# Kernel tuning notes

Hardware: AMD Instinct MI355X
Metric: run time of the kernel (lower is better)

The kernel has to match this reference:

```python
import jax, jax.numpy as jnp
import numpy as np

B = 1024      # molecules in batch
M = 128       # atoms per molecule
K = 32        # max_num_neighbors
CUTOFF = 5.0  # radius cutoff


def setup_inputs() -> dict:
    key = jax.random.key(0)
    pos = jax.random.normal(key, (B * M, 3), dtype=jnp.float32) * 3.0
    batch = (jnp.arange(B * M, dtype=jnp.int32) // M).astype(jnp.int32)
    return {"pos": pos, "batch": batch}


def reference(pos, batch):
    # pos: [N,3]; batch is sorted with M atoms per molecule -> reshape [B,M,3]
    p = pos.reshape(B, M, 3)
    sq = jnp.sum(p * p, axis=-1)  # [B,M]
    # per-molecule pairwise squared distances, [B,M,M]
    d2 = sq[:, :, None] + sq[:, None, :] - 2.0 * jnp.einsum('bic,bjc->bij', p, p)
    d2 = jnp.maximum(d2, 0.0)
    valid = d2 < CUTOFF * CUTOFF  # loop=True: self (d2=0) is included
    d2m = jnp.where(valid, d2, jnp.inf)
    neg, idx = jax.lax.top_k(-d2m, K)       # K nearest in-radius, idx: [B,M,K]
    taken = jnp.isfinite(neg)                # which slots are real edges
    local_i = jnp.arange(M, dtype=idx.dtype)
    idx = jnp.where(taken, idx, local_i[None, :, None])  # pad with self index

    # gather neighbor positions: [B,M,K,3]
    p_nb = p[jnp.arange(B)[:, None, None], idx]
    vec = p_nb - p[:, :, None, :]            # pos[edge0] - pos[edge1] (source - target)

    nonself = idx != local_i[None, :, None]
    mask = taken & nonself                   # self-loops & padding get weight 0
    sqv = jnp.sum(vec * vec, axis=-1)
    weight = jnp.where(mask, jnp.sqrt(jnp.where(mask, sqv, 1.0)), 0.0)

    node_base = (jnp.arange(B, dtype=jnp.int32) * M)[:, None, None]
    src = (node_base + idx.astype(jnp.int32)).reshape(-1)                 # edge_index[0] = neighbor j
    dst = jnp.broadcast_to(node_base + local_i.astype(jnp.int32)[None, :, None], (B, M, K)).reshape(-1)
    edge_index = jnp.stack([src, dst], axis=0)          # [2, B*M*K]
    edge_weight = weight.reshape(-1)                    # [B*M*K]
    edge_vec = vec.reshape(-1, 3)                       # [B*M*K, 3]
    return edge_index, edge_weight, edge_vec
```

## Files before the change

### kernel.cpp

```cpp
#include <hip/hip_runtime.h>
#include <stdint.h>

#define BB 1024
#define MM 128
#define KK 32
#define NEDGE (BB * MM * KK)
#define BPB 4
#define ROWS_PER_WAVE (MM / (4 * BPB))

typedef unsigned int uint2v __attribute__((ext_vector_type(2)));

static constexpr unsigned long long p1mask(int size, int stride) {
    unsigned long long m = 0;
    for (int l = 0; l < 64; ++l) {
        int g = l & 31;
        bool up = (((g & size) == 0) != (l >= 32));
        bool keep = (((g & stride) == 0) == up);
        if (keep) m |= 1ull << l;
    }
    return m;
}
static constexpr unsigned long long cleanmask(int stride) {
    unsigned long long m = 0;
    for (int l = 0; l < 64; ++l) {
        int g = l & 31;
        if ((g & stride) == 0) m |= 1ull << l;
    }
    return m;
}

template<int ST, unsigned long long MASK>
static __device__ __forceinline__ unsigned cex(unsigned k) {
    unsigned mn, mx, r;
    if constexpr (ST == 1) {
        asm("s_nop 1\n\t"
            "v_min_u32_dpp %0, %2, %2 quad_perm:[1,0,3,2] row_mask:0xf bank_mask:0xf\n\t"
            "v_max_u32_dpp %1, %2, %2 quad_perm:[1,0,3,2] row_mask:0xf bank_mask:0xf"
            : "=&v"(mn), "=&v"(mx) : "v"(k));
    } else if constexpr (ST == 2) {
        asm("s_nop 1\n\t"
            "v_min_u32_dpp %0, %2, %2 quad_perm:[2,3,0,1] row_mask:0xf bank_mask:0xf\n\t"
            "v_max_u32_dpp %1, %2, %2 quad_perm:[2,3,0,1] row_mask:0xf bank_mask:0xf"
            : "=&v"(mn), "=&v"(mx) : "v"(k));
    } else if constexpr (ST == 8) {
        asm("s_nop 1\n\t"
            "v_min_u32_dpp %0, %2, %2 row_ror:8 row_mask:0xf bank_mask:0xf\n\t"
            "v_max_u32_dpp %1, %2, %2 row_ror:8 row_mask:0xf bank_mask:0xf"
            : "=&v"(mn), "=&v"(mx) : "v"(k));
    } else {
        unsigned p = (unsigned)__builtin_amdgcn_ds_swizzle((int)k, (ST << 10) | 0x1F);
        mn = __builtin_elementwise_min(k, p);
        mx = __builtin_elementwise_max(k, p);
    }
    asm("v_cndmask_b32 %0, %1, %2, %3" : "=v"(r) : "v"(mx), "v"(mn), "s"(MASK));
    return r;
}

static __device__ __forceinline__ unsigned minxor32(unsigned k) {
#if __has_builtin(__builtin_amdgcn_permlane32_swap)
    uint2v s = __builtin_amdgcn_permlane32_swap(k, k, false, false);
    return __builtin_elementwise_min(s.x, s.y);
#else
    unsigned p = (unsigned)__shfl_xor((int)k, 32, 64);
    return __builtin_elementwise_min(k, p);
#endif
}

__global__ __launch_bounds__(256, 4) void knn_edges_kernel(const float* __restrict__ pos,
                                                           float* __restrict__ out) {
    __shared__ float px[MM], py[MM], pz[MM], sqs[MM];
    const int blk = blockIdx.x;
    const int b = blk >> 2;
    const int sub = blk & (BPB - 1);
    const int tid = threadIdx.x;

    if (tid < MM) {
        const float* p = pos + (size_t)(b * MM + tid) * 3;
        float x = p[0], y = p[1], z = p[2];
        px[tid] = x; py[tid] = y; pz[tid] = z;
        sqs[tid] = __fadd_rn(__fadd_rn(__fmul_rn(x, x), __fmul_rn(y, y)), __fmul_rn(z, z));
    }
    __syncthreads();

    const int wave = tid >> 6;
    const int lane = tid & 63;
    const int r = lane & 31;
    const bool hi = lane >= 32;

    const int j0 = lane, j1 = lane + 64;
    const float xa = px[j0], ya = py[j0], za = pz[j0], qa = sqs[j0];
    const float xb = px[j1], yb = py[j1], zb = pz[j1], qb = sqs[j1];

    const int row0 = sub * (MM / BPB) + wave * ROWS_PER_WAVE;
    const int node0 = b * MM + row0;
    const float fbase = (float)(b * MM);

    float* const vecbase = out + 3 * (size_t)NEDGE;
    const long e0 = (long)node0 * KK + r;
    float* pA = hi ? out + (size_t)NEDGE + e0 : out + e0;
    float* pB = hi ? out + 2 * (size_t)NEDGE + e0 : vecbase + e0 * 3;
    float* pC = hi ? vecbase + e0 * 3 + 2 : vecbase + e0 * 3 + 1;
    const int sA = KK;
    const int sB = hi ? KK : KK * 3;
    const int sC = KK * 3;

#pragma unroll 2
    for (int i = row0; i < row0 + ROWS_PER_WAVE; ++i) {
        const float xi = px[i], yi = py[i], zi = pz[i], qi = sqs[i];

        float dot0 = fmaf(xi, xa, fmaf(yi, ya, zi * za));
        float d20 = fmaxf((qi + qa) - 2.0f * dot0, 0.0f);
        unsigned k0 = (__float_as_uint(d20) & 0xFFFFFF80u) | (unsigned)j0;

        float dot1 = fmaf(xi, xb, fmaf(yi, yb, zi * zb));
        float d21 = fmaxf((qi + qb) - 2.0f * dot1, 0.0f);
        unsigned k1 = (__float_as_uint(d21) & 0xFFFFFF80u) | (unsigned)j1;

#define P1(S, ST) k0 = cex<ST, p1mask(S, ST)>(k0); k1 = cex<ST, p1mask(S, ST)>(k1);
        P1(2, 1)
        P1(4, 2)  P1(4, 1)
        P1(8, 4)  P1(8, 2)  P1(8, 1)
        P1(16, 8) P1(16, 4) P1(16, 2) P1(16, 1)
        P1(32, 16) P1(32, 8) P1(32, 4) P1(32, 2) P1(32, 1)
#undef P1

        unsigned c  = minxor32(k0);
        unsigned c2 = minxor32(k1);

#define P3(ST) c = cex<ST, cleanmask(ST)>(c); c2 = cex<ST, ~cleanmask(ST)>(c2);
        P3(16) P3(8) P3(4) P3(2) P3(1)
#undef P3

        unsigned m = __builtin_elementwise_min(c, c2);

#define P5(ST) m = cex<ST, cleanmask(ST)>(m);
        P5(16) P5(8) P5(4) P5(2) P5(1)
#undef P5

        const bool taken = m < 0x41C80000u;
        const int j = (int)(m & 127u);
        const int sel = taken ? j : i;

        float dxv = __fsub_rn(px[sel], xi);
        float dyv = __fsub_rn(py[sel], yi);
        float dzv = __fsub_rn(pz[sel], zi);
        float w = (taken && j != i)
                      ? sqrtf(__fadd_rn(__fadd_rn(__fmul_rn(dxv, dxv), __fmul_rn(dyv, dyv)),
                                        __fmul_rn(dzv, dzv)))
                      : 0.0f;

        const float fnode = (float)(b * MM + i);
        const float fsrc = fbase + (float)sel;

        *pA = hi ? fnode : fsrc;
        *pB = hi ? w : dxv;
        *pC = hi ? dzv : dyv;
        pA += sA; pB += sB; pC += sC;
    }
}

extern "C" void kernel_launch(void* const* d_in, const int* in_sizes, int n_in,
                              void* d_out, int out_size, void* d_ws, size_t ws_size,
                              hipStream_t stream) {
    const float* pos = (const float*)d_in[0];
    float* out = (float*)d_out;
    hipLaunchKernelGGL(knn_edges_kernel, dim3(BB * BPB), dim3(256), 0, stream, pos, out);
}
```

Before: 48.94 us.

## Restructure bitonic network with opposite-direction halves to merge and cut a stage

Sorts the two 64-key halves in opposite directions so they can be min-merged directly, which removes one full clean-up stage of the reduction network. Compare-exchanges are interleaved in paired inline asm so the DPP hazard s_nop is shared between the two keys. The mask/select for weight is dropped in favour of an unconditional sqrt of an fma sum, and the node index is computed incrementally. Both rely on self and padding producing zero distance, and the fma changes rounding of the weight compared with the reference's separate multiplies and adds.

```diff
diff --git a/kernel.cpp b/kernel.cpp
--- a/kernel.cpp
+++ b/kernel.cpp
@@ -20,6 +20,15 @@
     }
     return m;
 }
+static constexpr unsigned long long dualmask(int stride) {
+    unsigned long long m = 0;
+    for (int l = 0; l < 64; ++l) {
+        int g = l & 31;
+        bool km = (l < 32) ? ((g & stride) == 0) : ((g & stride) != 0);
+        if (km) m |= 1ull << l;
+    }
+    return m;
+}
 static constexpr unsigned long long cleanmask(int stride) {
     unsigned long long m = 0;
     for (int l = 0; l < 64; ++l) {
@@ -29,23 +38,56 @@
     return m;
 }
 
+#define DPP1 "quad_perm:[1,0,3,2] row_mask:0xf bank_mask:0xf"
+#define DPP2 "quad_perm:[2,3,0,1] row_mask:0xf bank_mask:0xf"
+#define DPP8 "row_ror:8 row_mask:0xf bank_mask:0xf"
+
+#define CEX2_DPP(DPPSTR, NOPSTR, S, ST)                                      \
+  { constexpr unsigned long long M0c = p1mask(S, ST);                        \
+    constexpr unsigned long long M1c = ~p1mask(S, ST);                       \
+    unsigned mn0, mx0, mn1, mx1, r0, r1;                                     \
+    asm(NOPSTR                                                               \
+        "v_min_u32_dpp %0, %6, %6 " DPPSTR "\n\t"                            \
+        "v_max_u32_dpp %1, %6, %6 " DPPSTR "\n\t"                            \
+        "v_min_u32_dpp %2, %7, %7 " DPPSTR "\n\t"                            \
+        "v_max_u32_dpp %3, %7, %7 " DPPSTR "\n\t"                            \
+        "v_cndmask_b32 %4, %1, %0, %8\n\t"                                   \
+        "v_cndmask_b32 %5, %3, %2, %9"                                       \
+        : "=&v"(mn0), "=&v"(mx0), "=&v"(mn1), "=&v"(mx1), "=&v"(r0), "=&v"(r1)\
+        : "v"(k0), "v"(k1), "s"(M0c), "s"(M1c));                             \
+    k0 = r0; k1 = r1; }
+
+#define CEX2_SW(ST, S)                                                       \
+  { constexpr unsigned long long M0c = p1mask(S, ST);                        \
+    constexpr unsigned long long M1c = ~p1mask(S, ST);                       \
+    unsigned p0 = (unsigned)__builtin_amdgcn_ds_swizzle((int)k0, ((ST) << 10) | 0x1F); \
+    unsigned p1 = (unsigned)__builtin_amdgcn_ds_swizzle((int)k1, ((ST) << 10) | 0x1F); \
+    unsigned mn0 = __builtin_elementwise_min(k0, p0);                        \
+    unsigned mx0 = __builtin_elementwise_max(k0, p0);                        \
+    unsigned mn1 = __builtin_elementwise_min(k1, p1);                        \
+    unsigned mx1 = __builtin_elementwise_max(k1, p1);                        \
+    unsigned r0, r1;                                                         \
+    asm("v_cndmask_b32 %0, %1, %2, %3" : "=v"(r0) : "v"(mx0), "v"(mn0), "s"(M0c)); \
+    asm("v_cndmask_b32 %0, %1, %2, %3" : "=v"(r1) : "v"(mx1), "v"(mn1), "s"(M1c)); \
+    k0 = r0; k1 = r1; }
+
 template<int ST, unsigned long long MASK>
-static __device__ __forceinline__ unsigned cex(unsigned k) {
+static __device__ __forceinline__ unsigned cex1(unsigned k) {
     unsigned mn, mx, r;
     if constexpr (ST == 1) {
         asm("s_nop 1\n\t"
-            "v_min_u32_dpp %0, %2, %2 quad_perm:[1,0,3,2] row_mask:0xf bank_mask:0xf\n\t"
-            "v_max_u32_dpp %1, %2, %2 quad_perm:[1,0,3,2] row_mask:0xf bank_mask:0xf"
+            "v_min_u32_dpp %0, %2, %2 " DPP1 "\n\t"
+            "v_max_u32_dpp %1, %2, %2 " DPP1
             : "=&v"(mn), "=&v"(mx) : "v"(k));
     } else if constexpr (ST == 2) {
         asm("s_nop 1\n\t"
-            "v_min_u32_dpp %0, %2, %2 quad_perm:[2,3,0,1] row_mask:0xf bank_mask:0xf\n\t"
-            "v_max_u32_dpp %1, %2, %2 quad_perm:[2,3,0,1] row_mask:0xf bank_mask:0xf"
+            "v_min_u32_dpp %0, %2, %2 " DPP2 "\n\t"
+            "v_max_u32_dpp %1, %2, %2 " DPP2
             : "=&v"(mn), "=&v"(mx) : "v"(k));
     } else if constexpr (ST == 8) {
         asm("s_nop 1\n\t"
-            "v_min_u32_dpp %0, %2, %2 row_ror:8 row_mask:0xf bank_mask:0xf\n\t"
-            "v_max_u32_dpp %1, %2, %2 row_ror:8 row_mask:0xf bank_mask:0xf"
+            "v_min_u32_dpp %0, %2, %2 " DPP8 "\n\t"
+            "v_max_u32_dpp %1, %2, %2 " DPP8
             : "=&v"(mn), "=&v"(mx) : "v"(k));
     } else {
         unsigned p = (unsigned)__builtin_amdgcn_ds_swizzle((int)k, (ST << 10) | 0x1F);
@@ -98,11 +140,11 @@
     float* const vecbase = out + 3 * (size_t)NEDGE;
     const long e0 = (long)node0 * KK + r;
     float* pA = hi ? out + (size_t)NEDGE + e0 : out + e0;
-    float* pB = hi ? out + 2 * (size_t)NEDGE + e0 : vecbase + e0 * 3;
-    float* pC = hi ? vecbase + e0 * 3 + 2 : vecbase + e0 * 3 + 1;
-    const int sA = KK;
-    const int sB = hi ? KK : KK * 3;
-    const int sC = KK * 3;
+    float* pB = vecbase + e0 * 3 + (hi ? 2 : 0);
+    float* pC = hi ? out + 2 * (size_t)NEDGE + e0 : vecbase + e0 * 3 + 1;
+    const int sC = hi ? KK : KK * 3;
+
+    float fnode = (float)node0;
 
 #pragma unroll 2
     for (int i = row0; i < row0 + ROWS_PER_WAVE; ++i) {
@@ -116,26 +158,37 @@
         float d21 = fmaxf((qi + qb) - 2.0f * dot1, 0.0f);
         unsigned k1 = (__float_as_uint(d21) & 0xFFFFFF80u) | (unsigned)j1;
 
-#define P1(S, ST) k0 = cex<ST, p1mask(S, ST)>(k0); k1 = cex<ST, p1mask(S, ST)>(k1);
-        P1(2, 1)
-        P1(4, 2)  P1(4, 1)
-        P1(8, 4)  P1(8, 2)  P1(8, 1)
-        P1(16, 8) P1(16, 4) P1(16, 2) P1(16, 1)
-        P1(32, 16) P1(32, 8) P1(32, 4) P1(32, 2) P1(32, 1)
-#undef P1
-
-        unsigned c  = minxor32(k0);
-        unsigned c2 = minxor32(k1);
-
-#define P3(ST) c = cex<ST, cleanmask(ST)>(c); c2 = cex<ST, ~cleanmask(ST)>(c2);
-        P3(16) P3(8) P3(4) P3(2) P3(1)
-#undef P3
-
-        unsigned m = __builtin_elementwise_min(c, c2);
-
-#define P5(ST) m = cex<ST, cleanmask(ST)>(m);
-        P5(16) P5(8) P5(4) P5(2) P5(1)
-#undef P5
+        CEX2_DPP(DPP1, "s_nop 1\n\t", 2, 1)
+        CEX2_DPP(DPP2, "",            4, 2)
+        CEX2_DPP(DPP1, "",            4, 1)
+        CEX2_SW(4,                    8)
+        CEX2_DPP(DPP2, "s_nop 1\n\t", 8, 2)
+        CEX2_DPP(DPP1, "",            8, 1)
+        CEX2_DPP(DPP8, "",            16, 8)
+        CEX2_SW(4,                    16)
+        CEX2_DPP(DPP2, "s_nop 1\n\t", 16, 2)
+        CEX2_DPP(DPP1, "",            16, 1)
+        CEX2_SW(16,                   32)
+        CEX2_DPP(DPP8, "s_nop 1\n\t", 32, 8)
+        CEX2_SW(4,                    32)
+        CEX2_DPP(DPP2, "s_nop 1\n\t", 32, 2)
+        CEX2_DPP(DPP1, "",            32, 1)
+
+        unsigned c = __builtin_elementwise_min(k0, k1);
+
+        c = cex1<16, dualmask(16)>(c);
+        c = cex1<8,  dualmask(8)>(c);
+        c = cex1<4,  dualmask(4)>(c);
+        c = cex1<2,  dualmask(2)>(c);
+        c = cex1<1,  dualmask(1)>(c);
+
+        unsigned m = minxor32(c);
+
+        m = cex1<16, cleanmask(16)>(m);
+        m = cex1<8,  cleanmask(8)>(m);
+        m = cex1<4,  cleanmask(4)>(m);
+        m = cex1<2,  cleanmask(2)>(m);
+        m = cex1<1,  cleanmask(1)>(m);
 
         const bool taken = m < 0x41C80000u;
         const int j = (int)(m & 127u);
@@ -144,18 +197,15 @@
         float dxv = __fsub_rn(px[sel], xi);
         float dyv = __fsub_rn(py[sel], yi);
         float dzv = __fsub_rn(pz[sel], zi);
-        float w = (taken && j != i)
-                      ? sqrtf(__fadd_rn(__fadd_rn(__fmul_rn(dxv, dxv), __fmul_rn(dyv, dyv)),
-                                        __fmul_rn(dzv, dzv)))
-                      : 0.0f;
-
-        const float fnode = (float)(b * MM + i);
+        float w = sqrtf(fmaf(dzv, dzv, fmaf(dyv, dyv, dxv * dxv)));
+
         const float fsrc = fbase + (float)sel;
 
         *pA = hi ? fnode : fsrc;
-        *pB = hi ? w : dxv;
-        *pC = hi ? dzv : dyv;
-        pA += sA; pB += sB; pC += sC;
+        *pB = hi ? dzv : dxv;
+        *pC = hi ? w : dyv;
+        pA += KK; pB += KK * 3; pC += sC;
+        fnode += 1.0f;
     }
 }
 
```

New measurement: 45.20 us. 1.08x faster.

## Interleave two rows per iteration and use XOR-direction bitonic sort with swizzles

Applied to the files above, without the earlier changes.

Each wave now processes two rows at once (four sort keys per lane) to expose more independent work and hide cross-lane latency. The bitonic direction is folded into the keys by XOR-ing per-lane masks, so every compare-exchange uses a fixed alternating SGPR mask, and the DPP variants are replaced by ds_swizzle. Weight computation drops the explicit self/taken check and relies on the vector being zero, and uses fmaf. This raises register pressure and puts more swizzle traffic through the LDS crossbar, and fmaf may change rounding slightly.

```diff
diff --git a/kernel.cpp b/kernel.cpp
--- a/kernel.cpp
+++ b/kernel.cpp
@@ -7,54 +7,15 @@
 #define NEDGE (BB * MM * KK)
 #define BPB 4
 #define ROWS_PER_WAVE (MM / (4 * BPB))
+#define HALF (ROWS_PER_WAVE / 2)
 
 typedef unsigned int uint2v __attribute__((ext_vector_type(2)));
 
-static constexpr unsigned long long p1mask(int size, int stride) {
-    unsigned long long m = 0;
-    for (int l = 0; l < 64; ++l) {
-        int g = l & 31;
-        bool up = (((g & size) == 0) != (l >= 32));
-        bool keep = (((g & stride) == 0) == up);
-        if (keep) m |= 1ull << l;
-    }
-    return m;
-}
-static constexpr unsigned long long cleanmask(int stride) {
-    unsigned long long m = 0;
-    for (int l = 0; l < 64; ++l) {
-        int g = l & 31;
-        if ((g & stride) == 0) m |= 1ull << l;
-    }
-    return m;
-}
-
-template<int ST, unsigned long long MASK>
-static __device__ __forceinline__ unsigned cex(unsigned k) {
-    unsigned mn, mx, r;
-    if constexpr (ST == 1) {
-        asm("s_nop 1\n\t"
-            "v_min_u32_dpp %0, %2, %2 quad_perm:[1,0,3,2] row_mask:0xf bank_mask:0xf\n\t"
-            "v_max_u32_dpp %1, %2, %2 quad_perm:[1,0,3,2] row_mask:0xf bank_mask:0xf"
-            : "=&v"(mn), "=&v"(mx) : "v"(k));
-    } else if constexpr (ST == 2) {
-        asm("s_nop 1\n\t"
-            "v_min_u32_dpp %0, %2, %2 quad_perm:[2,3,0,1] row_mask:0xf bank_mask:0xf\n\t"
-            "v_max_u32_dpp %1, %2, %2 quad_perm:[2,3,0,1] row_mask:0xf bank_mask:0xf"
-            : "=&v"(mn), "=&v"(mx) : "v"(k));
-    } else if constexpr (ST == 8) {
-        asm("s_nop 1\n\t"
-            "v_min_u32_dpp %0, %2, %2 row_ror:8 row_mask:0xf bank_mask:0xf\n\t"
-            "v_max_u32_dpp %1, %2, %2 row_ror:8 row_mask:0xf bank_mask:0xf"
-            : "=&v"(mn), "=&v"(mx) : "v"(k));
-    } else {
-        unsigned p = (unsigned)__builtin_amdgcn_ds_swizzle((int)k, (ST << 10) | 0x1F);
-        mn = __builtin_elementwise_min(k, p);
-        mx = __builtin_elementwise_max(k, p);
-    }
-    asm("v_cndmask_b32 %0, %1, %2, %3" : "=v"(r) : "v"(mx), "v"(mn), "s"(MASK));
-    return r;
-}
+#define CEXS(K, ST, MSK)                                                      \
+  { unsigned p_ = (unsigned)__builtin_amdgcn_ds_swizzle((int)(K), ((ST) << 10) | 0x1F); \
+    unsigned mn_ = __builtin_elementwise_min((K), p_);                        \
+    unsigned mx_ = __builtin_elementwise_max((K), p_);                        \
+    asm("v_cndmask_b32 %0, %1, %2, %3" : "=v"(K) : "v"(mx_), "v"(mn_), "s"(MSK)); }
 
 static __device__ __forceinline__ unsigned minxor32(unsigned k) {
 #if __has_builtin(__builtin_amdgcn_permlane32_swap)
@@ -84,78 +45,122 @@
 
     const int wave = tid >> 6;
     const int lane = tid & 63;
-    const int r = lane & 31;
+    const int g = lane & 31;
     const bool hi = lane >= 32;
+    const unsigned upper = hi ? ~0u : 0u;
+
+    unsigned long long m1  = 0x5555555555555555ull;
+    unsigned long long m2  = 0x3333333333333333ull;
+    unsigned long long m4  = 0x0F0F0F0F0F0F0F0Full;
+    unsigned long long m8  = 0x00FF00FF00FF00FFull;
+    unsigned long long m16 = 0x0000FFFF0000FFFFull;
+    asm("" : "+s"(m1), "+s"(m2), "+s"(m4), "+s"(m8), "+s"(m16));
+
+    auto dmask = [&](int s) -> unsigned {
+        unsigned zer = ((g & s) == 0) ? ~0u : 0u;
+        return ~(zer ^ upper);
+    };
+    const unsigned f2    = dmask(2);
+    const unsigned nf2   = ~f2;
+    const unsigned f4c   = dmask(4);
+    const unsigned f8c   = dmask(8);
+    const unsigned f16c  = dmask(16);
+    const unsigned f32c  = dmask(32);
+    const unsigned t24   = f2 ^ f4c;
+    const unsigned t48   = f4c ^ f8c;
+    const unsigned t816  = f8c ^ f16c;
+    const unsigned t1632 = f16c ^ f32c;
+    const unsigned nf32  = ~f32c;
 
     const int j0 = lane, j1 = lane + 64;
     const float xa = px[j0], ya = py[j0], za = pz[j0], qa = sqs[j0];
     const float xb = px[j1], yb = py[j1], zb = pz[j1], qb = sqs[j1];
 
     const int row0 = sub * (MM / BPB) + wave * ROWS_PER_WAVE;
-    const int node0 = b * MM + row0;
     const float fbase = (float)(b * MM);
 
     float* const vecbase = out + 3 * (size_t)NEDGE;
-    const long e0 = (long)node0 * KK + r;
+    const long e0 = (long)(b * MM + row0) * KK + g;
     float* pA = hi ? out + (size_t)NEDGE + e0 : out + e0;
-    float* pB = hi ? out + 2 * (size_t)NEDGE + e0 : vecbase + e0 * 3;
-    float* pC = hi ? vecbase + e0 * 3 + 2 : vecbase + e0 * 3 + 1;
-    const int sA = KK;
-    const int sB = hi ? KK : KK * 3;
-    const int sC = KK * 3;
+    float* pB = vecbase + e0 * 3 + (hi ? 2 : 0);
+    float* pC = hi ? out + 2 * (size_t)NEDGE + e0 : vecbase + e0 * 3 + 1;
+    const int sC = hi ? KK : 3 * KK;
+    const int oC = sC * HALF;
 
-#pragma unroll 2
-    for (int i = row0; i < row0 + ROWS_PER_WAVE; ++i) {
-        const float xi = px[i], yi = py[i], zi = pz[i], qi = sqs[i];
+    for (int ii = 0; ii < HALF; ++ii) {
+        const int ia = row0 + ii;
+        const int ib = ia + HALF;
 
-        float dot0 = fmaf(xi, xa, fmaf(yi, ya, zi * za));
-        float d20 = fmaxf((qi + qa) - 2.0f * dot0, 0.0f);
-        unsigned k0 = (__float_as_uint(d20) & 0xFFFFFF80u) | (unsigned)j0;
+        const float xia = px[ia], yia = py[ia], zia = pz[ia], qia = sqs[ia];
+        const float xib = px[ib], yib = py[ib], zib = pz[ib], qib = sqs[ib];
 
-        float dot1 = fmaf(xi, xb, fmaf(yi, yb, zi * zb));
-        float d21 = fmaxf((qi + qb) - 2.0f * dot1, 0.0f);
-        unsigned k1 = (__float_as_uint(d21) & 0xFFFFFF80u) | (unsigned)j1;
+        float dot;
+        dot = fmaf(xia, xa, fmaf(yia, ya, zia * za));
+        unsigned K0a = ((__float_as_uint(fmaxf(fmaf(-2.0f, dot, qia + qa), 0.0f)) & 0xFFFFFF80u) | (unsigned)j0) ^ f2;
+        dot = fmaf(xia, xb, fmaf(yia, yb, zia * zb));
+        unsigned K1a = ((__float_as_uint(fmaxf(fmaf(-2.0f, dot, qia + qb), 0.0f)) & 0xFFFFFF80u) | (unsigned)j1) ^ nf2;
+        dot = fmaf(xib, xa, fmaf(yib, ya, zib * za));
+        unsigned K0b = ((__float_as_uint(fmaxf(fmaf(-2.0f, dot, qib + qa), 0.0f)) & 0xFFFFFF80u) | (unsigned)j0) ^ f2;
+        dot = fmaf(xib, xb, fmaf(yib, yb, zib * zb));
+        unsigned K1b = ((__float_as_uint(fmaxf(fmaf(-2.0f, dot, qib + qb), 0.0f)) & 0xFFFFFF80u) | (unsigned)j1) ^ nf2;
 
-#define P1(S, ST) k0 = cex<ST, p1mask(S, ST)>(k0); k1 = cex<ST, p1mask(S, ST)>(k1);
-        P1(2, 1)
-        P1(4, 2)  P1(4, 1)
-        P1(8, 4)  P1(8, 2)  P1(8, 1)
-        P1(16, 8) P1(16, 4) P1(16, 2) P1(16, 1)
-        P1(32, 16) P1(32, 8) P1(32, 4) P1(32, 2) P1(32, 1)
-#undef P1
+#define ST4(ST, MSK) CEXS(K0a, ST, MSK) CEXS(K1a, ST, MSK) CEXS(K0b, ST, MSK) CEXS(K1b, ST, MSK)
+#define XOR4(V) K0a ^= (V); K1a ^= (V); K0b ^= (V); K1b ^= (V);
 
-        unsigned c  = minxor32(k0);
-        unsigned c2 = minxor32(k1);
+        ST4(1, m1)
+        XOR4(t24)
+        ST4(2, m2) ST4(1, m1)
+        XOR4(t48)
+        ST4(4, m4) ST4(2, m2) ST4(1, m1)
+        XOR4(t816)
+        ST4(8, m8) ST4(4, m4) ST4(2, m2) ST4(1, m1)
+        XOR4(t1632)
+        ST4(16, m16) ST4(8, m8) ST4(4, m4) ST4(2, m2) ST4(1, m1)
+#undef ST4
+#undef XOR4
 
-#define P3(ST) c = cex<ST, cleanmask(ST)>(c); c2 = cex<ST, ~cleanmask(ST)>(c2);
-        P3(16) P3(8) P3(4) P3(2) P3(1)
-#undef P3
+        unsigned Ca = (__builtin_elementwise_min(K0a ^ f32c, K1a ^ nf32)) ^ upper;
+        unsigned Cb = (__builtin_elementwise_min(K0b ^ f32c, K1b ^ nf32)) ^ upper;
 
-        unsigned m = __builtin_elementwise_min(c, c2);
+#define CS2(ST, MSK) CEXS(Ca, ST, MSK) CEXS(Cb, ST, MSK)
+        CS2(16, m16) CS2(8, m8) CS2(4, m4) CS2(2, m2) CS2(1, m1)
+#undef CS2
 
-#define P5(ST) m = cex<ST, cleanmask(ST)>(m);
-        P5(16) P5(8) P5(4) P5(2) P5(1)
-#undef P5
+        unsigned Ma = minxor32(Ca ^ upper);
+        unsigned Mb = minxor32(Cb ^ upper);
+#define MS2(ST, MSK) CEXS(Ma, ST, MSK) CEXS(Mb, ST, MSK)
+        MS2(16, m16) MS2(8, m8) MS2(4, m4) MS2(2, m2) MS2(1, m1)
+#undef MS2
 
-        const bool taken = m < 0x41C80000u;
-        const int j = (int)(m & 127u);
-        const int sel = taken ? j : i;
-
-        float dxv = __fsub_rn(px[sel], xi);
-        float dyv = __fsub_rn(py[sel], yi);
-        float dzv = __fsub_rn(pz[sel], zi);
-        float w = (taken && j != i)
-                      ? sqrtf(__fadd_rn(__fadd_rn(__fmul_rn(dxv, dxv), __fmul_rn(dyv, dyv)),
-                                        __fmul_rn(dzv, dzv)))
-                      : 0.0f;
-
-        const float fnode = (float)(b * MM + i);
-        const float fsrc = fbase + (float)sel;
-
-        *pA = hi ? fnode : fsrc;
-        *pB = hi ? w : dxv;
-        *pC = hi ? dzv : dyv;
-        pA += sA; pB += sB; pC += sC;
+        {
+            const bool taken = Ma < 0x41C80000u;
+            const int j = (int)(Ma & 127u);
+            const int sel = taken ? j : ia;
+            float dxv = __fsub_rn(px[sel], xia);
+            float dyv = __fsub_rn(py[sel], yia);
+            float dzv = __fsub_rn(pz[sel], zia);
+            float w = sqrtf(fmaf(dzv, dzv, fmaf(dyv, dyv, dxv * dxv)));
+            const float fsrc = fbase + (float)sel;
+            const float fnode = fbase + (float)ia;
+            pA[0] = hi ? fnode : fsrc;
+            pB[0] = hi ? dzv : dxv;
+            pC[0] = hi ? w : dyv;
+        }
+        {
+            const bool taken = Mb < 0x41C80000u;
+            const int j = (int)(Mb & 127u);
+            const int sel = taken ? j : ib;
+            float dxv = __fsub_rn(px[sel], xib);
+            float dyv = __fsub_rn(py[sel], yib);
+            float dzv = __fsub_rn(pz[sel], zib);
+            float w = sqrtf(fmaf(dzv, dzv, fmaf(dyv, dyv, dxv * dxv)));
+            const float fsrc = fbase + (float)sel;
+            const float fnode = fbase + (float)ib;
+            pA[HALF * KK] = hi ? fnode : fsrc;
+            pB[HALF * 3 * KK] = hi ? dzv : dxv;
+            pC[oC] = hi ? w : dyv;
+        }
+        pA += KK; pB += 3 * KK; pC += sC;
     }
 }
 
```

Result: faster. 46.50 us (-5.0%).
